# Kernel tuning notes

Hardware: AMD Instinct MI355X
Metric: run time of the kernel (lower is better)

Reference implementation:

```python
import math
import jax, jax.numpy as jnp
import numpy as np

LLM = 4096
QB = 512
SAM = 256
H = W = 64
OUT = 256
HEADS = 4
DH = SAM // HEADS
EPS = 1e-5


def _ln(x, g, b):
    mu = jnp.mean(x, axis=-1, keepdims=True)
    var = jnp.mean(jnp.square(x - mu), axis=-1, keepdims=True)
    return (x - mu) * jax.lax.rsqrt(var + EPS) * g + b


def _conv3x3(x, w):
    # x: (N,C,H,W), w: (O,I,3,3), padding=1
    return jax.lax.conv_general_dilated(
        x, w, window_strides=(1, 1), padding='SAME',
        dimension_numbers=('NCHW', 'OIHW', 'NCHW'))


def setup_inputs() -> dict:
    key = jax.random.key(0)
    ks = jax.random.split(key, 20)
    n = lambda k, sh, s: (jax.random.normal(k, sh, dtype=jnp.float32) * s)
    inp = {
        'image_embed': n(ks[0], (8, SAM, H, W), 1.0),
        'ref_vec': n(ks[1], (8, 32, LLM), 1.0),
        'querybook_slots': n(ks[2], (8, 32, QB), 1.0),
        # parameters (torch Linear layout: (out, in); conv: (O,I,kh,kw))
        'q_proj_w': n(ks[3], (HEADS * DH, LLM), 1.0 / math.sqrt(LLM)),
        'k_proj_w': n(ks[4], (HEADS * DH, SAM, 1, 1), 1.0 / math.sqrt(SAM)),
        'fuser_w1': n(ks[5], (HEADS, HEADS, 3, 3), 1.0 / math.sqrt(HEADS * 9)),
        'fuser_b1': n(ks[6], (HEADS,), 0.01),
        'fuser_w2': n(ks[7], (1, HEADS, 3, 3), 1.0 / math.sqrt(HEADS * 9)),
        'fuser_b2': jnp.full((1,), -1.8, dtype=jnp.float32),
        'qb_proj_w': n(ks[8], (LLM, QB), 1.0 / math.sqrt(QB)),
        'rf_ln_g': jnp.ones((2 * LLM,), jnp.float32),
        'rf_ln_b': jnp.zeros((2 * LLM,), jnp.float32),
        'rf_lin_w': n(ks[9], (LLM, 2 * LLM), 1.0 / math.sqrt(2 * LLM)),
        'rf_lin_b': n(ks[10], (LLM,), 0.01),
        'cf_ln_g': jnp.ones((LLM,), jnp.float32),
        'cf_ln_b': jnp.zeros((LLM,), jnp.float32),
        'cf_w1': n(ks[11], (LLM // 2, LLM), 1.0 / math.sqrt(LLM)),
        'cf_b1': n(ks[12], (LLM // 2,), 0.01),
        'cf_w2': n(ks[13], (1, LLM // 2), 1.0 / math.sqrt(LLM // 2)),
        'cf_b2': n(ks[14], (1,), 0.01),
    }
    return inp


def reference(image_embed, ref_vec, querybook_slots, q_proj_w, k_proj_w,
              fuser_w1, fuser_b1, fuser_w2, fuser_b2, qb_proj_w,
              rf_ln_g, rf_ln_b, rf_lin_w, rf_lin_b,
              cf_ln_g, cf_ln_b, cf_w1, cf_b1, cf_w2, cf_b2):
    B, C, h, w = image_embed.shape
    K = ref_vec.shape[1]
    # querybook projection + ref fuse
    qb = jnp.einsum('bkq,lq->bkl', querybook_slots, qb_proj_w)  # (B,K,LLM)
    cat = jnp.concatenate([ref_vec, qb], axis=-1)               # (B,K,2*LLM)
    fused = jax.nn.silu(jnp.einsum('bkc,lc->bkl', _ln(cat, rf_ln_g, rf_ln_b), rf_lin_w) + rf_lin_b)
    # per-slot query heads
    Q = jnp.einsum('bkl,ol->bko', fused, q_proj_w).reshape(B, K, HEADS, DH)
    # 1x1 conv key map -> (B,HEADS,DH,H,W)
    Kmap = jnp.einsum('bcxy,oc->boxy', image_embed, k_proj_w.reshape(HEADS * DH, SAM))
    Kmap = Kmap.reshape(B, HEADS, DH, h, w)
    # fused contraction over d_head (original materialized (B,K,HEADS,DH,H,W))
    logits_64_heads = jnp.einsum('bkhd,bhdxy->bkhxy', Q, Kmap) / math.sqrt(DH)
    x = logits_64_heads.reshape(B * K, HEADS, h, w)
    x = jax.nn.silu(_conv3x3(x, fuser_w1) + fuser_b1[None, :, None, None])
    logits_64 = _conv3x3(x, fuser_w2) + fuser_b2[None, :, None, None]  # (B*K,1,64,64)
    # bilinear upsample, align_corners=False (half-pixel centers)
    up = jax.image.resize(logits_64, (B * K, 1, OUT, OUT), method='bilinear')
    ref_logits_256 = up.reshape(B, K, OUT, OUT)
    # confidence head
    cfh = jax.nn.silu(jnp.einsum('bkl,ol->bko', _ln(fused, cf_ln_g, cf_ln_b), cf_w1) + cf_b1)
    conf_logits = (jnp.einsum('bko,lo->bkl', cfh, cf_w2) + cf_b2).squeeze(-1)  # (B,K)
    return ref_logits_256, conf_logits
```

## Files before the change

### kernel.cpp

```cpp
#include <hip/hip_runtime.h>

#define EPS 1e-5f

typedef __bf16 bf16_t;
typedef __bf16 bf16x8 __attribute__((ext_vector_type(8)));
typedef __bf16 bf16x4 __attribute__((ext_vector_type(4)));
typedef float f32x4 __attribute__((ext_vector_type(4)));

__device__ __forceinline__ float silu_f(float x) { return x / (1.f + __expf(-x)); }

__device__ __forceinline__ float block_sum(float v, float* tmp) {
#pragma unroll
  for (int off = 32; off > 0; off >>= 1) v += __shfl_down(v, off);
  __syncthreads();
  if ((threadIdx.x & 63) == 0) tmp[threadIdx.x >> 6] = v;
  __syncthreads();
  return tmp[0] + tmp[1] + tmp[2] + tmp[3];
}

__global__ __launch_bounds__(1024, 4) void gemm_wide(
    const bf16_t* __restrict__ A, const float* __restrict__ B,
    bf16_t* __restrict__ Cpart, int N, int K, int KS) {
  __shared__ bf16_t As[256][72];
  __shared__ bf16_t Bs[128][72];
  const int t = threadIdx.x;
  const int lane = t & 63;
  const int w = t >> 6;
  const int n0 = blockIdx.x * 128;
  const int kbeg = blockIdx.y * KS;
  const int nt = KS >> 6;
  const int ar = t >> 2, ac = (t & 3) * 16;
  const int br = t >> 3, bc = (t & 7) * 8;
  const bf16_t* Ap = A + (size_t)ar * K + kbeg + ac;
  const float* Bp = B + (size_t)(n0 + br) * K + kbeg + bc;

  bf16x8 a0A, a1A, a0B, a1B, a0C, a1C, a0D, a1D;
  float4 b0A, b1A, b0B, b1B, b0C, b1C, b0D, b1D;

#define LOADSET(S, k0)                            \
  a0##S = *(const bf16x8*)(Ap + (k0));            \
  a1##S = *(const bf16x8*)(Ap + (k0) + 8);        \
  b0##S = *(const float4*)(Bp + (k0));            \
  b1##S = *(const float4*)(Bp + (k0) + 4);

#define STORESET(S)                                                         \
  {                                                                         \
    *(bf16x8*)&As[ar][ac] = a0##S;                                          \
    *(bf16x8*)&As[ar][ac + 8] = a1##S;                                      \
    bf16x8 wv;                                                              \
    wv[0] = (bf16_t)b0##S.x; wv[1] = (bf16_t)b0##S.y;                       \
    wv[2] = (bf16_t)b0##S.z; wv[3] = (bf16_t)b0##S.w;                       \
    wv[4] = (bf16_t)b1##S.x; wv[5] = (bf16_t)b1##S.y;                       \
    wv[6] = (bf16_t)b1##S.z; wv[7] = (bf16_t)b1##S.w;                       \
    *(bf16x8*)&Bs[br][bc] = wv;                                             \
  }

#define BARRIER_PINNED                 \
  __builtin_amdgcn_sched_barrier(0);   \
  __builtin_amdgcn_s_barrier();        \
  __builtin_amdgcn_sched_barrier(0);

#define LGKM_BARRIER                                   \
  asm volatile("s_waitcnt lgkmcnt(0)" ::: "memory");   \
  BARRIER_PINNED

  f32x4 acc[4][2];
#pragma unroll
  for (int i = 0; i < 4; ++i)
#pragma unroll
    for (int j = 0; j < 2; ++j) acc[i][j] = f32x4{0.f, 0.f, 0.f, 0.f};

  const int wm = (w & 3) * 64;
  const int wn = (w >> 2) * 32;
  const int fr = lane & 15;
  const int kq = (lane >> 4) * 8;

  auto COMPUTE = [&]() {
#pragma unroll
    for (int kk = 0; kk < 64; kk += 32) {
      bf16x8 af[4], bg[2];
#pragma unroll
      for (int i = 0; i < 4; ++i)
        af[i] = *(const bf16x8*)&As[wm + 16 * i + fr][kk + kq];
#pragma unroll
      for (int j = 0; j < 2; ++j)
        bg[j] = *(const bf16x8*)&Bs[wn + 16 * j + fr][kk + kq];
#pragma unroll
      for (int i = 0; i < 4; ++i)
#pragma unroll
        for (int j = 0; j < 2; ++j)
          acc[i][j] = __builtin_amdgcn_mfma_f32_16x16x32_bf16(af[i], bg[j], acc[i][j], 0, 0, 0);
    }
  };

#define PHASE(s_, SET)                                         \
  COMPUTE();                                                   \
  BARRIER_PINNED                                               \
  if ((s_) + 1 < nt) { STORESET(SET) }                         \
  if ((s_) + 5 < nt) { LOADSET(SET, ((s_) + 5) * 64) }         \
  LGKM_BARRIER

  LOADSET(A, 0)
  LOADSET(B, 64)
  LOADSET(C, 128)
  LOADSET(D, 192)
  STORESET(A)
  if (4 < nt) { LOADSET(A, 256) }
  LGKM_BARRIER

  for (int s = 0; s < nt; s += 4) {
    PHASE(s, B)
    PHASE(s + 1, C)
    PHASE(s + 2, D)
    PHASE(s + 3, A)
  }
#undef LOADSET
#undef STORESET
#undef PHASE

  bf16_t* Cz = Cpart + (size_t)blockIdx.y * 256 * N;
  const int rh = (lane >> 4) * 4, col = lane & 15;
#pragma unroll
  for (int i = 0; i < 4; ++i)
#pragma unroll
    for (int j = 0; j < 2; ++j)
#pragma unroll
      for (int rr = 0; rr < 4; ++rr)
        Cz[(size_t)(wm + 16 * i + rh + rr) * N + n0 + wn + 16 * j + col] =
            (bf16_t)acc[i][j][rr];
}

__global__ __launch_bounds__(1024) void gemm_wide_s(
    const float* __restrict__ A, const float* __restrict__ B,
    bf16_t* __restrict__ Cpart, int N, int K, int KS) {
  __shared__ bf16_t As[256][72];
  __shared__ bf16_t Bs[128][72];
  const int t = threadIdx.x;
  const int lane = t & 63;
  const int w = t >> 6;
  const int n0 = blockIdx.x * 128;
  const int kbeg = blockIdx.y * KS;
  const int nt = KS >> 6;
  const int ar = t >> 2, ac = (t & 3) * 16;
  const int br = t >> 3, bc = (t & 7) * 8;
  const float* Ap = A + (size_t)ar * K + kbeg + ac;
  const float* Bp = B + (size_t)(n0 + br) * K + kbeg + bc;

  f32x4 acc[4][2];
#pragma unroll
  for (int i = 0; i < 4; ++i)
#pragma unroll
    for (int j = 0; j < 2; ++j) acc[i][j] = f32x4{0.f, 0.f, 0.f, 0.f};

  const int wm = (w & 3) * 64;
  const int wn = (w >> 2) * 32;
  const int fr = lane & 15;
  const int kq = (lane >> 4) * 8;

  for (int s = 0; s < nt; ++s) {
    float4 av[4], bv[2];
#pragma unroll
    for (int i = 0; i < 4; ++i) av[i] = *(const float4*)(Ap + s * 64 + 4 * i);
#pragma unroll
    for (int i = 0; i < 2; ++i) bv[i] = *(const float4*)(Bp + s * 64 + 4 * i);
    __syncthreads();
    {
      bf16x8 wa0, wa1, wb;
      wa0[0] = (bf16_t)av[0].x; wa0[1] = (bf16_t)av[0].y; wa0[2] = (bf16_t)av[0].z; wa0[3] = (bf16_t)av[0].w;
      wa0[4] = (bf16_t)av[1].x; wa0[5] = (bf16_t)av[1].y; wa0[6] = (bf16_t)av[1].z; wa0[7] = (bf16_t)av[1].w;
      wa1[0] = (bf16_t)av[2].x; wa1[1] = (bf16_t)av[2].y; wa1[2] = (bf16_t)av[2].z; wa1[3] = (bf16_t)av[2].w;
      wa1[4] = (bf16_t)av[3].x; wa1[5] = (bf16_t)av[3].y; wa1[6] = (bf16_t)av[3].z; wa1[7] = (bf16_t)av[3].w;
      wb[0] = (bf16_t)bv[0].x; wb[1] = (bf16_t)bv[0].y; wb[2] = (bf16_t)bv[0].z; wb[3] = (bf16_t)bv[0].w;
      wb[4] = (bf16_t)bv[1].x; wb[5] = (bf16_t)bv[1].y; wb[6] = (bf16_t)bv[1].z; wb[7] = (bf16_t)bv[1].w;
      *(bf16x8*)&As[ar][ac] = wa0;
      *(bf16x8*)&As[ar][ac + 8] = wa1;
      *(bf16x8*)&Bs[br][bc] = wb;
    }
    __syncthreads();
#pragma unroll
    for (int kk = 0; kk < 64; kk += 32) {
      bf16x8 af[4], bg[2];
#pragma unroll
      for (int i = 0; i < 4; ++i)
        af[i] = *(const bf16x8*)&As[wm + 16 * i + fr][kk + kq];
#pragma unroll
      for (int j = 0; j < 2; ++j)
        bg[j] = *(const bf16x8*)&Bs[wn + 16 * j + fr][kk + kq];
#pragma unroll
      for (int i = 0; i < 4; ++i)
#pragma unroll
        for (int j = 0; j < 2; ++j)
          acc[i][j] = __builtin_amdgcn_mfma_f32_16x16x32_bf16(af[i], bg[j], acc[i][j], 0, 0, 0);
    }
    __syncthreads();
  }

  bf16_t* Cz = Cpart + (size_t)blockIdx.y * 256 * N;
  const int rh = (lane >> 4) * 4, col = lane & 15;
#pragma unroll
  for (int i = 0; i < 4; ++i)
#pragma unroll
    for (int j = 0; j < 2; ++j)
#pragma unroll
      for (int rr = 0; rr < 4; ++rr)
        Cz[(size_t)(wm + 16 * i + rh + rr) * N + n0 + wn + 16 * j + col] =
            (bf16_t)acc[i][j][rr];
}

__global__ __launch_bounds__(256) void gemm_small(
    const bf16_t* __restrict__ A16, const float* __restrict__ B32, float* __restrict__ Cv,
    int M, int N, int K, int KS, int S) {
  __shared__ bf16_t As[64][72];
  __shared__ bf16_t Bs[64][72];
  const int t = threadIdx.x;
  const int lane = t & 63;
  const int w = t >> 6;
  const int s = blockIdx.z;
  const int n0 = blockIdx.x * 64;
  const int m0 = blockIdx.y * 64;
  const int kbeg = s * KS;

  f32x4 acc[2][2];
#pragma unroll
  for (int i = 0; i < 2; ++i)
#pragma unroll
    for (int j = 0; j < 2; ++j) acc[i][j] = f32x4{0.f, 0.f, 0.f, 0.f};

  const int wm = (w & 1) * 32, wn = (w >> 1) * 32;
  const int fr = lane & 15;
  const int kq = (lane >> 4) * 8;

  for (int k0 = kbeg; k0 < kbeg + KS; k0 += 64) {
    bf16x8 a8[2];
    float4 b4[4];
    {
      const int rr = t >> 2, c8 = (t & 3) * 8;
#pragma unroll
      for (int i = 0; i < 2; ++i)
        a8[i] = *(const bf16x8*)(A16 + (size_t)(m0 + rr) * K + k0 + c8 + 32 * i);
    }
    {
      const int rr = t >> 4, c4 = (t & 15) * 4;
#pragma unroll
      for (int i = 0; i < 4; ++i)
        b4[i] = *(const float4*)(B32 + (size_t)(n0 + rr + 16 * i) * K + k0 + c4);
    }
    __syncthreads();
    {
      const int rr = t >> 2, c8 = (t & 3) * 8;
#pragma unroll
      for (int i = 0; i < 2; ++i) *(bf16x8*)&As[rr][c8 + 32 * i] = a8[i];
    }
    {
      const int rr = t >> 4, c4 = (t & 15) * 4;
#pragma unroll
      for (int i = 0; i < 4; ++i) {
        bf16x4 v = {(bf16_t)b4[i].x, (bf16_t)b4[i].y, (bf16_t)b4[i].z, (bf16_t)b4[i].w};
        *(bf16x4*)&Bs[rr + 16 * i][c4] = v;
      }
    }
    __syncthreads();
#pragma unroll
    for (int kk = 0; kk < 64; kk += 32) {
      bf16x8 af[2], bg[2];
#pragma unroll
      for (int i = 0; i < 2; ++i) {
        af[i] = *(const bf16x8*)&As[wm + 16 * i + fr][kk + kq];
        bg[i] = *(const bf16x8*)&Bs[wn + 16 * i + fr][kk + kq];
      }
#pragma unroll
      for (int i = 0; i < 2; ++i)
#pragma unroll
        for (int j = 0; j < 2; ++j)
          acc[i][j] = __builtin_amdgcn_mfma_f32_16x16x32_bf16(af[i], bg[j], acc[i][j], 0, 0, 0);
    }
    __syncthreads();
  }

  const int rh = (lane >> 4) * 4;
  const int col = lane & 15;
#pragma unroll
  for (int i = 0; i < 2; ++i)
#pragma unroll
    for (int j = 0; j < 2; ++j)
#pragma unroll
      for (int rr = 0; rr < 4; ++rr)
        Cv[(size_t)s * M * N + (size_t)(m0 + wm + 16 * i + rh + rr) * N + n0 + wn + 16 * j + col] =
            acc[i][j][rr];
}

__global__ __launch_bounds__(512) void gemm_attn(
    const float* __restrict__ A, const float* __restrict__ B, bf16_t* __restrict__ C) {
  __shared__ bf16_t As[128][72];
  __shared__ bf16_t Bs[64][72];
  const int t = threadIdx.x;
  const int lane = t & 63;
  const int w = t >> 6;
  const int b = blockIdx.y;
  const int n0 = blockIdx.x * 64;
  const float* Ab = A + (size_t)b * 32768;
  const float* Bb = B + (size_t)b * 1048576;

  f32x4 acc[2][2];
#pragma unroll
  for (int i = 0; i < 2; ++i)
#pragma unroll
    for (int j = 0; j < 2; ++j) acc[i][j] = f32x4{0.f, 0.f, 0.f, 0.f};

  const int wm = (w & 3) * 32;
  const int wn = (w >> 2) * 32;
  const int fr = lane & 15;
  const int kq = (lane >> 4) * 8;

  for (int k0 = 0; k0 < 256; k0 += 64) {
    const int r = t >> 2, c4 = (t & 3) * 16;
    float4 a4[4];
#pragma unroll
    for (int i = 0; i < 4; ++i)
      a4[i] = *(const float4*)(Ab + (size_t)r * 256 + k0 + c4 + 4 * i);
    const int kr = t >> 3, nc = (t & 7) * 8;
    float4 b4[2];
#pragma unroll
    for (int i = 0; i < 2; ++i)
      b4[i] = *(const float4*)(Bb + (size_t)(k0 + kr) * 4096 + n0 + nc + 4 * i);
    __syncthreads();
#pragma unroll
    for (int i = 0; i < 4; ++i) {
      bf16x4 v = {(bf16_t)a4[i].x, (bf16_t)a4[i].y, (bf16_t)a4[i].z, (bf16_t)a4[i].w};
      *(bf16x4*)&As[r][c4 + 4 * i] = v;
    }
#pragma unroll
    for (int i = 0; i < 2; ++i) {
      Bs[nc + 4 * i + 0][kr] = (bf16_t)b4[i].x;
      Bs[nc + 4 * i + 1][kr] = (bf16_t)b4[i].y;
      Bs[nc + 4 * i + 2][kr] = (bf16_t)b4[i].z;
      Bs[nc + 4 * i + 3][kr] = (bf16_t)b4[i].w;
    }
    __syncthreads();
#pragma unroll
    for (int kk = 0; kk < 64; kk += 32) {
      bf16x8 af[2], bg[2];
#pragma unroll
      for (int i = 0; i < 2; ++i) {
        af[i] = *(const bf16x8*)&As[wm + 16 * i + fr][kk + kq];
        bg[i] = *(const bf16x8*)&Bs[wn + 16 * i + fr][kk + kq];
      }
#pragma unroll
      for (int i = 0; i < 2; ++i)
#pragma unroll
        for (int j = 0; j < 2; ++j)
          acc[i][j] = __builtin_amdgcn_mfma_f32_16x16x32_bf16(af[i], bg[j], acc[i][j], 0, 0, 0);
    }
    __syncthreads();
  }

  bf16_t* Cb = C + (size_t)b * 524288;
  const int rh = (lane >> 4) * 4, col = lane & 15;
#pragma unroll
  for (int i = 0; i < 2; ++i)
#pragma unroll
    for (int j = 0; j < 2; ++j)
#pragma unroll
      for (int rr = 0; rr < 4; ++rr)
        Cb[(size_t)(wm + 16 * i + rh + rr) * 4096 + n0 + wn + 16 * j + col] =
            (bf16_t)acc[i][j][rr];
}

template <int SILU_, int BIAS_>
__global__ __launch_bounds__(256) void reduce_b(
    const bf16_t* __restrict__ part, int S, long slice,
    const float* __restrict__ bias, float scale,
    float* __restrict__ outF, bf16_t* __restrict__ outB,
    long nmask, long total8) {
  long i8 = (long)blockIdx.x * 256 + threadIdx.x;
  if (i8 >= total8) return;
  long i = i8 * 8;
  float a[8] = {0.f, 0.f, 0.f, 0.f, 0.f, 0.f, 0.f, 0.f};
  for (int s = 0; s < S; ++s) {
    bf16x8 v = *(const bf16x8*)(part + (size_t)s * slice + i);
#pragma unroll
    for (int j = 0; j < 8; ++j) a[j] += (float)v[j];
  }
#pragma unroll
  for (int j = 0; j < 8; ++j) a[j] *= scale;
  if (BIAS_) {
    const float* bb = bias + (i & nmask);
#pragma unroll
    for (int j = 0; j < 8; ++j) a[j] += bb[j];
  }
  if (SILU_) {
#pragma unroll
    for (int j = 0; j < 8; ++j) a[j] = silu_f(a[j]);
  }
  if (outF) {
    float4 o0 = {a[0], a[1], a[2], a[3]}, o1 = {a[4], a[5], a[6], a[7]};
    *(float4*)(outF + i) = o0;
    *(float4*)(outF + i + 4) = o1;
  }
  if (outB) {
    bf16x8 o;
#pragma unroll
    for (int j = 0; j < 8; ++j) o[j] = (bf16_t)a[j];
    *(bf16x8*)(outB + i) = o;
  }
}

__global__ __launch_bounds__(256) void reduce_k(
    const float* __restrict__ part, int S, long slice, float scale,
    float* __restrict__ outF, long total4) {
  long i4 = (long)blockIdx.x * 256 + threadIdx.x;
  if (i4 >= total4) return;
  long i = i4 * 4;
  float4 v = *(const float4*)(part + i);
  for (int s = 1; s < S; ++s) {
    float4 u = *(const float4*)(part + (size_t)s * slice + i);
    v.x += u.x; v.y += u.y; v.z += u.z; v.w += u.w;
  }
  v.x *= scale; v.y *= scale; v.z *= scale; v.w *= scale;
  *(float4*)(outF + i) = v;
}

__global__ __launch_bounds__(256) void ln_rows(
    const float* __restrict__ X1, const float* __restrict__ X2, int L1, int L2,
    const float* __restrict__ g, const float* __restrict__ bta, bf16_t* __restrict__ Y) {
  __shared__ float tmp[4];
  const int row = blockIdx.x;
  const int L = L1 + L2;
  const float* x1 = X1 + (size_t)row * L1;
  const float* x2 = X2 ? X2 + (size_t)row * L2 : nullptr;
  float s = 0.f, ss = 0.f;
  for (int i = threadIdx.x * 4; i < L1; i += 1024) {
    float4 v = *(const float4*)(x1 + i);
    s += v.x + v.y + v.z + v.w;
    ss += v.x * v.x + v.y * v.y + v.z * v.z + v.w * v.w;
  }
  for (int i = threadIdx.x * 4; i < L2; i += 1024) {
    float4 v = *(const float4*)(x2 + i);
    s += v.x + v.y + v.z + v.w;
    ss += v.x * v.x + v.y * v.y + v.z * v.z + v.w * v.w;
  }
  s = block_sum(s, tmp);
  ss = block_sum(ss, tmp);
  const float mu = s / (float)L;
  const float inv = rsqrtf(ss / (float)L - mu * mu + EPS);
  bf16_t* y = Y + (size_t)row * L;
  for (int i = threadIdx.x * 4; i < L1; i += 1024) {
    float4 v = *(const float4*)(x1 + i);
    float4 gv = *(const float4*)(g + i);
    float4 bv = *(const float4*)(bta + i);
    bf16x4 o = {(bf16_t)((v.x - mu) * inv * gv.x + bv.x),
                (bf16_t)((v.y - mu) * inv * gv.y + bv.y),
                (bf16_t)((v.z - mu) * inv * gv.z + bv.z),
                (bf16_t)((v.w - mu) * inv * gv.w + bv.w)};
    *(bf16x4*)(y + i) = o;
  }
  for (int i = threadIdx.x * 4; i < L2; i += 1024) {
    float4 v = *(const float4*)(x2 + i);
    float4 gv = *(const float4*)(g + L1 + i);
    float4 bv = *(const float4*)(bta + L1 + i);
    bf16x4 o = {(bf16_t)((v.x - mu) * inv * gv.x + bv.x),
                (bf16_t)((v.y - mu) * inv * gv.y + bv.y),
                (bf16_t)((v.z - mu) * inv * gv.z + bv.z),
                (bf16_t)((v.w - mu) * inv * gv.w + bv.w)};
    *(bf16x4*)(y + L1 + i) = o;
  }
}

__global__ __launch_bounds__(256) void qw_kernel(
    const float* __restrict__ Q, const float* __restrict__ kW, float* __restrict__ QW) {
  __shared__ float q[256];
  const int bk = blockIdx.x;
  q[threadIdx.x] = Q[(size_t)bk * 256 + threadIdx.x];
  __syncthreads();
  const int c = threadIdx.x;
#pragma unroll
  for (int h = 0; h < 4; ++h) {
    float s = 0.f;
#pragma unroll 8
    for (int d = 0; d < 64; ++d)
      s += q[(h << 6) + d] * kW[(size_t)(((h << 6) + d) << 8) + c];
    QW[((size_t)(bk * 4 + h) << 8) + c] = s;
  }
}

__global__ __launch_bounds__(256) void conv_fused(
    const bf16_t* __restrict__ X, const float* __restrict__ W1,
    const float* __restrict__ B1, const float* __restrict__ W2,
    const float* __restrict__ B2, float* __restrict__ O) {
  __shared__ bf16_t lg[16384];
  __shared__ bf16_t mid[16384];
  __shared__ float lg64[4096];
  __shared__ float wsh[180];
  const int t = threadIdx.x;
  const size_t base = (size_t)blockIdx.x * 16384;
#pragma unroll
  for (int i = 0; i < 8; ++i) {
    int o = (i * 256 + t) * 8;
    *(bf16x8*)&lg[o] = *(const bf16x8*)(X + base + o);
  }
  if (t < 144) wsh[t] = W1[t];
  else if (t < 180) wsh[t] = W2[t - 144];
  __syncthreads();
  const int px0 = (t & 15) * 4, py0 = (t >> 4) * 4;
  {
    float acc1[4][16];
#pragma unroll
    for (int oc = 0; oc < 4; ++oc) {
      float bb = B1[oc];
#pragma unroll
      for (int p = 0; p < 16; ++p) acc1[oc][p] = bb;
    }
#pragma unroll
    for (int c = 0; c < 4; ++c) {
      float p[6][6];
#pragma unroll
      for (int yy = 0; yy < 6; ++yy) {
        int gy = py0 + yy - 1;
#pragma unroll
        for (int xx = 0; xx < 6; ++xx) {
          int gx = px0 + xx - 1;
          p[yy][xx] = ((unsigned)gy < 64u && (unsigned)gx < 64u)
                          ? (float)lg[c * 4096 + gy * 64 + gx] : 0.f;
        }
      }
#pragma unroll
      for (int oc = 0; oc < 4; ++oc) {
        float wr[9];
#pragma unroll
        for (int k = 0; k < 9; ++k) wr[k] = wsh[oc * 36 + c * 9 + k];
#pragma unroll
        for (int y = 0; y < 4; ++y)
#pragma unroll
          for (int x = 0; x < 4; ++x)
            acc1[oc][y * 4 + x] +=
                wr[0] * p[y][x] + wr[1] * p[y][x + 1] + wr[2] * p[y][x + 2]
              + wr[3] * p[y + 1][x] + wr[4] * p[y + 1][x + 1] + wr[5] * p[y + 1][x + 2]
              + wr[6] * p[y + 2][x] + wr[7] * p[y + 2][x + 1] + wr[8] * p[y + 2][x + 2];
      }
    }
#pragma unroll
    for (int oc = 0; oc < 4; ++oc)
#pragma unroll
      for (int y = 0; y < 4; ++y) {
        bf16x4 o;
#pragma unroll
        for (int x = 0; x < 4; ++x) o[x] = (bf16_t)silu_f(acc1[oc][y * 4 + x]);
        *(bf16x4*)&mid[oc * 4096 + (py0 + y) * 64 + px0] = o;
      }
  }
  __syncthreads();
  {
    float acc2[16];
    float bb = B2[0];
#pragma unroll
    for (int p = 0; p < 16; ++p) acc2[p] = bb;
#pragma unroll
    for (int c = 0; c < 4; ++c) {
      float p[6][6];
#pragma unroll
      for (int yy = 0; yy < 6; ++yy) {
        int gy = py0 + yy - 1;
#pragma unroll
        for (int xx = 0; xx < 6; ++xx) {
          int gx = px0 + xx - 1;
          p[yy][xx] = ((unsigned)gy < 64u && (unsigned)gx < 64u)
                          ? (float)mid[c * 4096 + gy * 64 + gx] : 0.f;
        }
      }
      float wr[9];
#pragma unroll
      for (int k = 0; k < 9; ++k) wr[k] = wsh[144 + c * 9 + k];
#pragma unroll
      for (int y = 0; y < 4; ++y)
#pragma unroll
        for (int x = 0; x < 4; ++x)
          acc2[y * 4 + x] +=
              wr[0] * p[y][x] + wr[1] * p[y][x + 1] + wr[2] * p[y][x + 2]
            + wr[3] * p[y + 1][x] + wr[4] * p[y + 1][x + 1] + wr[5] * p[y + 1][x + 2]
            + wr[6] * p[y + 2][x] + wr[7] * p[y + 2][x + 1] + wr[8] * p[y + 2][x + 2];
    }
#pragma unroll
    for (int y = 0; y < 4; ++y)
#pragma unroll
      for (int x = 0; x < 4; ++x) lg64[(py0 + y) * 64 + px0 + x] = acc2[y * 4 + x];
  }
  __syncthreads();
  float* Ob = O + (size_t)blockIdx.x * 65536;
  for (int rr = 0; rr < 64; ++rr) {
    int p4 = rr * 256 + t;
    int oy = p4 >> 6, ox0 = (p4 & 63) * 4;
    float sy = oy * 0.25f - 0.375f;
    int y0 = (int)floorf(sy);
    float wy = sy - (float)y0;
    int y1 = min(y0 + 1, 63); y0 = max(y0, 0);
    const float* r0 = &lg64[y0 * 64];
    const float* r1 = &lg64[y1 * 64];
    float4 o;
#pragma unroll
    for (int q = 0; q < 4; ++q) {
      int ox = ox0 + q;
      float sx = ox * 0.25f - 0.375f;
      int x0 = (int)floorf(sx);
      float wx = sx - (float)x0;
      int x1 = min(x0 + 1, 63); x0 = max(x0, 0);
      float v0 = r0[x0] + wx * (r0[x1] - r0[x0]);
      float v1 = r1[x0] + wx * (r1[x1] - r1[x0]);
      ((float*)&o)[q] = v0 + wy * (v1 - v0);
    }
    *(float4*)(Ob + oy * 256 + ox0) = o;
  }
}

__global__ __launch_bounds__(256) void conf_k(
    const float* __restrict__ cfh, const float* __restrict__ w2,
    const float* __restrict__ b2, float* __restrict__ out) {
  __shared__ float tmp[4];
  const int row = blockIdx.x;
  float s = 0.f;
  for (int i = threadIdx.x; i < 2048; i += 256)
    s += cfh[(size_t)row * 2048 + i] * w2[i];
  s = block_sum(s, tmp);
  if (threadIdx.x == 0) out[row] = s + b2[0];
}

extern "C" void kernel_launch(void* const* d_in, const int* in_sizes, int n_in,
                              void* d_out, int out_size, void* d_ws, size_t ws_size,
                              hipStream_t stream) {
  const float* img    = (const float*)d_in[0];
  const float* refv   = (const float*)d_in[1];
  const float* qs     = (const float*)d_in[2];
  const float* qpw    = (const float*)d_in[3];
  const float* kpw    = (const float*)d_in[4];
  const float* fw1    = (const float*)d_in[5];
  const float* fb1    = (const float*)d_in[6];
  const float* fw2    = (const float*)d_in[7];
  const float* fb2    = (const float*)d_in[8];
  const float* qbw    = (const float*)d_in[9];
  const float* rlg    = (const float*)d_in[10];
  const float* rlb    = (const float*)d_in[11];
  const float* rlw    = (const float*)d_in[12];
  const float* rlbias = (const float*)d_in[13];
  const float* clg    = (const float*)d_in[14];
  const float* clb    = (const float*)d_in[15];
  const float* cw1    = (const float*)d_in[16];
  const float* cb1    = (const float*)d_in[17];
  const float* cw2    = (const float*)d_in[18];
  const float* cb2    = (const float*)d_in[19];
  float* out = (float*)d_out;
  char* W = (char*)d_ws;

  bf16_t* partF = (bf16_t*)(W + 0);
  bf16_t* l64hb = (bf16_t*)(W + 0);
  bf16_t* partC = (bf16_t*)(W + 0);
  bf16_t* catln = (bf16_t*)(W + 16777216);
  float*  fus   = (float*)(W + 16777216);
  float*  qbf   = (float*)(W + 20971520);
  bf16_t* fusb  = (bf16_t*)(W + 20971520);
  bf16_t* lnf   = (bf16_t*)(W + 20971520);
  bf16_t* partQ = (bf16_t*)(W + 25165824);
  float*  part8 = (float*)(W + 25165824);
  float*  Qb    = (float*)(W + 44040192);
  float*  QW    = (float*)(W + 44302336);
  float*  cfh   = (float*)(W + 45350912);

  dim3 b256(256);

  gemm_wide_s<<<dim3(32, 8), dim3(1024), 0, stream>>>(qs, qbw, partQ, 4096, 512, 64);
  reduce_b<0, 0><<<dim3(512), b256, 0, stream>>>(
      partQ, 8, 1048576L, nullptr, 1.f, qbf, nullptr, 0L, 131072L);
  ln_rows<<<dim3(256), b256, 0, stream>>>(refv, qbf, 4096, 4096, rlg, rlb, catln);
  gemm_wide<<<dim3(32, 8), dim3(1024), 0, stream>>>(catln, rlw, partF, 4096, 8192, 1024);
  reduce_b<1, 1><<<dim3(512), b256, 0, stream>>>(
      partF, 8, 1048576L, rlbias, 1.f, fus, fusb, 4095L, 131072L);
  gemm_small<<<dim3(4, 4, 8), b256, 0, stream>>>(fusb, qpw, part8, 256, 256, 4096, 512, 8);
  reduce_k<<<dim3(64), b256, 0, stream>>>(part8, 8, 65536L, 0.125f, Qb, 16384L);
  qw_kernel<<<dim3(256), b256, 0, stream>>>(Qb, kpw, QW);
  gemm_attn<<<dim3(64, 8), dim3(512), 0, stream>>>(QW, img, l64hb);
  conv_fused<<<dim3(256), b256, 0, stream>>>(l64hb, fw1, fb1, fw2, fb2, out);
  ln_rows<<<dim3(256), b256, 0, stream>>>(fus, nullptr, 4096, 0, clg, clb, lnf);
  gemm_wide<<<dim3(16, 16), dim3(1024), 0, stream>>>(lnf, cw1, partC, 2048, 4096, 256);
  reduce_b<1, 1><<<dim3(256), b256, 0, stream>>>(
      partC, 16, 524288L, cb1, 1.f, cfh, nullptr, 2047L, 65536L);
  conf_k<<<dim3(256), b256, 0, stream>>>(cfh, cw2, cb2, out + 16777216);
}
```

Before: 195.0 us.

## Double-buffer gemm_wide LDS and fold split-K reductions into LN and QW kernels

```diff
diff --git a/kernel.cpp b/kernel.cpp
--- a/kernel.cpp
+++ b/kernel.cpp
@@ -18,11 +18,11 @@
   return tmp[0] + tmp[1] + tmp[2] + tmp[3];
 }
 
-__global__ __launch_bounds__(1024, 4) void gemm_wide(
+__global__ __launch_bounds__(1024) void gemm_wide(
     const bf16_t* __restrict__ A, const float* __restrict__ B,
     bf16_t* __restrict__ Cpart, int N, int K, int KS) {
-  __shared__ bf16_t As[256][72];
-  __shared__ bf16_t Bs[128][72];
+  __shared__ bf16_t As[2][256][72];
+  __shared__ bf16_t Bs[2][128][72];
   const int t = threadIdx.x;
   const int lane = t & 63;
   const int w = t >> 6;
@@ -34,8 +34,8 @@
   const bf16_t* Ap = A + (size_t)ar * K + kbeg + ac;
   const float* Bp = B + (size_t)(n0 + br) * K + kbeg + bc;
 
-  bf16x8 a0A, a1A, a0B, a1B, a0C, a1C, a0D, a1D;
-  float4 b0A, b1A, b0B, b1B, b0C, b1C, b0D, b1D;
+  bf16x8 a0X, a1X, a0Y, a1Y, a0Z, a1Z;
+  float4 b0X, b1X, b0Y, b1Y, b0Z, b1Z;
 
 #define LOADSET(S, k0)                            \
   a0##S = *(const bf16x8*)(Ap + (k0));            \
@@ -43,26 +43,17 @@
   b0##S = *(const float4*)(Bp + (k0));            \
   b1##S = *(const float4*)(Bp + (k0) + 4);
 
-#define STORESET(S)                                                         \
+#define STORESET(S, buf)                                                    \
   {                                                                         \
-    *(bf16x8*)&As[ar][ac] = a0##S;                                          \
-    *(bf16x8*)&As[ar][ac + 8] = a1##S;                                      \
+    *(bf16x8*)&As[buf][ar][ac] = a0##S;                                     \
+    *(bf16x8*)&As[buf][ar][ac + 8] = a1##S;                                 \
     bf16x8 wv;                                                              \
     wv[0] = (bf16_t)b0##S.x; wv[1] = (bf16_t)b0##S.y;                       \
     wv[2] = (bf16_t)b0##S.z; wv[3] = (bf16_t)b0##S.w;                       \
     wv[4] = (bf16_t)b1##S.x; wv[5] = (bf16_t)b1##S.y;                       \
     wv[6] = (bf16_t)b1##S.z; wv[7] = (bf16_t)b1##S.w;                       \
-    *(bf16x8*)&Bs[br][bc] = wv;                                             \
-  }
-
-#define BARRIER_PINNED                 \
-  __builtin_amdgcn_sched_barrier(0);   \
-  __builtin_amdgcn_s_barrier();        \
-  __builtin_amdgcn_sched_barrier(0);
-
-#define LGKM_BARRIER                                   \
-  asm volatile("s_waitcnt lgkmcnt(0)" ::: "memory");   \
-  BARRIER_PINNED
+    *(bf16x8*)&Bs[buf][br][bc] = wv;                                        \
+  }
 
   f32x4 acc[4][2];
 #pragma unroll
@@ -75,16 +66,16 @@
   const int fr = lane & 15;
   const int kq = (lane >> 4) * 8;
 
-  auto COMPUTE = [&]() {
+  auto COMPUTE = [&](int buf) {
 #pragma unroll
     for (int kk = 0; kk < 64; kk += 32) {
       bf16x8 af[4], bg[2];
 #pragma unroll
       for (int i = 0; i < 4; ++i)
-        af[i] = *(const bf16x8*)&As[wm + 16 * i + fr][kk + kq];
+        af[i] = *(const bf16x8*)&As[buf][wm + 16 * i + fr][kk + kq];
 #pragma unroll
       for (int j = 0; j < 2; ++j)
-        bg[j] = *(const bf16x8*)&Bs[wn + 16 * j + fr][kk + kq];
+        bg[j] = *(const bf16x8*)&Bs[buf][wn + 16 * j + fr][kk + kq];
 #pragma unroll
       for (int i = 0; i < 4; ++i)
 #pragma unroll
@@ -93,30 +84,40 @@
     }
   };
 
-#define PHASE(s_, SET)                                         \
-  COMPUTE();                                                   \
-  BARRIER_PINNED                                               \
-  if ((s_) + 1 < nt) { STORESET(SET) }                         \
-  if ((s_) + 5 < nt) { LOADSET(SET, ((s_) + 5) * 64) }         \
-  LGKM_BARRIER
-
-  LOADSET(A, 0)
-  LOADSET(B, 64)
-  LOADSET(C, 128)
-  LOADSET(D, 192)
-  STORESET(A)
-  if (4 < nt) { LOADSET(A, 256) }
-  LGKM_BARRIER
-
-  for (int s = 0; s < nt; s += 4) {
-    PHASE(s, B)
-    PHASE(s + 1, C)
-    PHASE(s + 2, D)
-    PHASE(s + 3, A)
+#define SB __builtin_amdgcn_sched_barrier(0);
+#define END_PHASE                                      \
+  asm volatile("s_waitcnt lgkmcnt(0)" ::: "memory");   \
+  SB __builtin_amdgcn_s_barrier(); SB
+
+#define PHASE(s_, LS, SS, bufc)                              \
+  if ((s_) < nt) {                                           \
+    if ((s_) + 3 < nt) { LOADSET(LS, ((s_) + 3) * 64) }      \
+    SB                                                       \
+    if ((s_) + 1 < nt) { STORESET(SS, bufc ^ 1) }            \
+    COMPUTE(bufc);                                           \
+    END_PHASE                                                \
+  }
+
+  LOADSET(X, 0)
+  if (1 < nt) { LOADSET(Y, 64) }
+  if (2 < nt) { LOADSET(Z, 128) }
+  SB
+  STORESET(X, 0)
+  END_PHASE
+
+  for (int s6 = 0; s6 < nt; s6 += 6) {
+    PHASE(s6 + 0, X, Y, 0)
+    PHASE(s6 + 1, Y, Z, 1)
+    PHASE(s6 + 2, Z, X, 0)
+    PHASE(s6 + 3, X, Y, 1)
+    PHASE(s6 + 4, Y, Z, 0)
+    PHASE(s6 + 5, Z, X, 1)
   }
 #undef LOADSET
 #undef STORESET
 #undef PHASE
+#undef END_PHASE
+#undef SB
 
   bf16_t* Cz = Cpart + (size_t)blockIdx.y * 256 * N;
   const int rh = (lane >> 4) * 4, col = lane & 15;
@@ -405,45 +406,72 @@
   }
 }
 
-__global__ __launch_bounds__(256) void reduce_k(
-    const float* __restrict__ part, int S, long slice, float scale,
-    float* __restrict__ outF, long total4) {
-  long i4 = (long)blockIdx.x * 256 + threadIdx.x;
-  if (i4 >= total4) return;
-  long i = i4 * 4;
-  float4 v = *(const float4*)(part + i);
-  for (int s = 1; s < S; ++s) {
-    float4 u = *(const float4*)(part + (size_t)s * slice + i);
-    v.x += u.x; v.y += u.y; v.z += u.z; v.w += u.w;
-  }
-  v.x *= scale; v.y *= scale; v.z *= scale; v.w *= scale;
-  *(float4*)(outF + i) = v;
-}
-
-__global__ __launch_bounds__(256) void ln_rows(
-    const float* __restrict__ X1, const float* __restrict__ X2, int L1, int L2,
+__global__ __launch_bounds__(256) void ln_fuse(
+    const float* __restrict__ refv, const bf16_t* __restrict__ partQ, int S,
     const float* __restrict__ g, const float* __restrict__ bta, bf16_t* __restrict__ Y) {
   __shared__ float tmp[4];
   const int row = blockIdx.x;
-  const int L = L1 + L2;
+  const int t = threadIdx.x;
+  const long i0 = t * 16;
+  float q[16];
+#pragma unroll
+  for (int j = 0; j < 16; ++j) q[j] = 0.f;
+  for (int s = 0; s < S; ++s) {
+    const bf16_t* p = partQ + (size_t)s * 1048576 + (size_t)row * 4096 + i0;
+    bf16x8 v0 = *(const bf16x8*)(p);
+    bf16x8 v1 = *(const bf16x8*)(p + 8);
+#pragma unroll
+    for (int j = 0; j < 8; ++j) { q[j] += (float)v0[j]; q[8 + j] += (float)v1[j]; }
+  }
+  const float* xr = refv + (size_t)row * 4096 + i0;
+  float r[16];
+#pragma unroll
+  for (int j = 0; j < 4; ++j) {
+    float4 v = *(const float4*)(xr + 4 * j);
+    r[4 * j] = v.x; r[4 * j + 1] = v.y; r[4 * j + 2] = v.z; r[4 * j + 3] = v.w;
+  }
+  float s1 = 0.f, s2 = 0.f;
+#pragma unroll
+  for (int j = 0; j < 16; ++j) { s1 += r[j] + q[j]; s2 += r[j] * r[j] + q[j] * q[j]; }
+  s1 = block_sum(s1, tmp);
+  s2 = block_sum(s2, tmp);
+  const float mu = s1 / 8192.f;
+  const float inv = rsqrtf(s2 / 8192.f - mu * mu + EPS);
+  bf16_t* y = Y + (size_t)row * 8192;
+  bf16x8 o0, o1;
+#pragma unroll
+  for (int j = 0; j < 8; ++j) {
+    o0[j] = (bf16_t)((r[j] - mu) * inv * g[i0 + j] + bta[i0 + j]);
+    o1[j] = (bf16_t)((r[8 + j] - mu) * inv * g[i0 + 8 + j] + bta[i0 + 8 + j]);
+  }
+  *(bf16x8*)(y + i0) = o0;
+  *(bf16x8*)(y + i0 + 8) = o1;
+#pragma unroll
+  for (int j = 0; j < 8; ++j) {
+    o0[j] = (bf16_t)((q[j] - mu) * inv * g[4096 + i0 + j] + bta[4096 + i0 + j]);
+    o1[j] = (bf16_t)((q[8 + j] - mu) * inv * g[4096 + i0 + 8 + j] + bta[4096 + i0 + 8 + j]);
+  }
+  *(bf16x8*)(y + 4096 + i0) = o0;
+  *(bf16x8*)(y + 4096 + i0 + 8) = o1;
+}
+
+__global__ __launch_bounds__(256) void ln_rows(
+    const float* __restrict__ X1, int L1,
+    const float* __restrict__ g, const float* __restrict__ bta, bf16_t* __restrict__ Y) {
+  __shared__ float tmp[4];
+  const int row = blockIdx.x;
   const float* x1 = X1 + (size_t)row * L1;
-  const float* x2 = X2 ? X2 + (size_t)row * L2 : nullptr;
   float s = 0.f, ss = 0.f;
   for (int i = threadIdx.x * 4; i < L1; i += 1024) {
     float4 v = *(const float4*)(x1 + i);
     s += v.x + v.y + v.z + v.w;
     ss += v.x * v.x + v.y * v.y + v.z * v.z + v.w * v.w;
   }
-  for (int i = threadIdx.x * 4; i < L2; i += 1024) {
-    float4 v = *(const float4*)(x2 + i);
-    s += v.x + v.y + v.z + v.w;
-    ss += v.x * v.x + v.y * v.y + v.z * v.z + v.w * v.w;
-  }
   s = block_sum(s, tmp);
   ss = block_sum(ss, tmp);
-  const float mu = s / (float)L;
-  const float inv = rsqrtf(ss / (float)L - mu * mu + EPS);
-  bf16_t* y = Y + (size_t)row * L;
+  const float mu = s / (float)L1;
+  const float inv = rsqrtf(ss / (float)L1 - mu * mu + EPS);
+  bf16_t* y = Y + (size_t)row * L1;
   for (int i = threadIdx.x * 4; i < L1; i += 1024) {
     float4 v = *(const float4*)(x1 + i);
     float4 gv = *(const float4*)(g + i);
@@ -454,25 +482,18 @@
                 (bf16_t)((v.w - mu) * inv * gv.w + bv.w)};
     *(bf16x4*)(y + i) = o;
   }
-  for (int i = threadIdx.x * 4; i < L2; i += 1024) {
-    float4 v = *(const float4*)(x2 + i);
-    float4 gv = *(const float4*)(g + L1 + i);
-    float4 bv = *(const float4*)(bta + L1 + i);
-    bf16x4 o = {(bf16_t)((v.x - mu) * inv * gv.x + bv.x),
-                (bf16_t)((v.y - mu) * inv * gv.y + bv.y),
-                (bf16_t)((v.z - mu) * inv * gv.z + bv.z),
-                (bf16_t)((v.w - mu) * inv * gv.w + bv.w)};
-    *(bf16x4*)(y + L1 + i) = o;
-  }
-}
-
-__global__ __launch_bounds__(256) void qw_kernel(
-    const float* __restrict__ Q, const float* __restrict__ kW, float* __restrict__ QW) {
+}
+
+__global__ __launch_bounds__(256) void qw_fuse(
+    const float* __restrict__ part8, const float* __restrict__ kW, float* __restrict__ QW) {
   __shared__ float q[256];
   const int bk = blockIdx.x;
-  q[threadIdx.x] = Q[(size_t)bk * 256 + threadIdx.x];
+  const int c = threadIdx.x;
+  float sq = 0.f;
+#pragma unroll
+  for (int s = 0; s < 8; ++s) sq += part8[(size_t)s * 65536 + (size_t)bk * 256 + c];
+  q[c] = 0.125f * sq;
   __syncthreads();
-  const int c = threadIdx.x;
 #pragma unroll
   for (int h = 0; h < 4; ++h) {
     float s = 0.f;
@@ -649,35 +670,30 @@
   float* out = (float*)d_out;
   char* W = (char*)d_ws;
 
+  bf16_t* partQ = (bf16_t*)(W + 0);
   bf16_t* partF = (bf16_t*)(W + 0);
   bf16_t* l64hb = (bf16_t*)(W + 0);
   bf16_t* partC = (bf16_t*)(W + 0);
   bf16_t* catln = (bf16_t*)(W + 16777216);
   float*  fus   = (float*)(W + 16777216);
-  float*  qbf   = (float*)(W + 20971520);
   bf16_t* fusb  = (bf16_t*)(W + 20971520);
   bf16_t* lnf   = (bf16_t*)(W + 20971520);
-  bf16_t* partQ = (bf16_t*)(W + 25165824);
-  float*  part8 = (float*)(W + 25165824);
-  float*  Qb    = (float*)(W + 44040192);
-  float*  QW    = (float*)(W + 44302336);
-  float*  cfh   = (float*)(W + 45350912);
+  float*  part8 = (float*)(W + 23068672);
+  float*  QW    = (float*)(W + 25165824);
+  float*  cfh   = (float*)(W + 26214400);
 
   dim3 b256(256);
 
   gemm_wide_s<<<dim3(32, 8), dim3(1024), 0, stream>>>(qs, qbw, partQ, 4096, 512, 64);
-  reduce_b<0, 0><<<dim3(512), b256, 0, stream>>>(
-      partQ, 8, 1048576L, nullptr, 1.f, qbf, nullptr, 0L, 131072L);
-  ln_rows<<<dim3(256), b256, 0, stream>>>(refv, qbf, 4096, 4096, rlg, rlb, catln);
+  ln_fuse<<<dim3(256), b256, 0, stream>>>(refv, partQ, 8, rlg, rlb, catln);
   gemm_wide<<<dim3(32, 8), dim3(1024), 0, stream>>>(catln, rlw, partF, 4096, 8192, 1024);
   reduce_b<1, 1><<<dim3(512), b256, 0, stream>>>(
       partF, 8, 1048576L, rlbias, 1.f, fus, fusb, 4095L, 131072L);
   gemm_small<<<dim3(4, 4, 8), b256, 0, stream>>>(fusb, qpw, part8, 256, 256, 4096, 512, 8);
-  reduce_k<<<dim3(64), b256, 0, stream>>>(part8, 8, 65536L, 0.125f, Qb, 16384L);
-  qw_kernel<<<dim3(256), b256, 0, stream>>>(Qb, kpw, QW);
+  qw_fuse<<<dim3(256), b256, 0, stream>>>(part8, kpw, QW);
   gemm_attn<<<dim3(64, 8), dim3(512), 0, stream>>>(QW, img, l64hb);
   conv_fused<<<dim3(256), b256, 0, stream>>>(l64hb, fw1, fb1, fw2, fb2, out);
-  ln_rows<<<dim3(256), b256, 0, stream>>>(fus, nullptr, 4096, 0, clg, clb, lnf);
+  ln_rows<<<dim3(256), b256, 0, stream>>>(fus, 4096, clg, clb, lnf);
   gemm_wide<<<dim3(16, 16), dim3(1024), 0, stream>>>(lnf, cw1, partC, 2048, 4096, 256);
   reduce_b<1, 1><<<dim3(256), b256, 0, stream>>>(
       partC, 16, 524288L, cb1, 1.f, cfh, nullptr, 2047L, 65536L);
```

Result: faster. 187.9 us (-3.7%).
